# Kernel optimization log

Measured on AMD Instinct MI355X. Metric: run time of the kernel, lower is better.

## Reference

```python
import jax, jax.numpy as jnp
import numpy as np

INF = 1e8
SAMPLE_RATE = 22050.0
DOWNSAMPLE = 256.0
TARGET_RATE = SAMPLE_RATE / DOWNSAMPLE  # ~86.13 frames/sec
BEAT_RADIUS = 2.5
DOWNBEAT_RADIUS = 4.5
CLUSTERS = np.array([0.35, 0.7, 1.4, 2.8, 5.6], dtype=np.float64)

def _interval_length_ranges():
    # clusters_to_interval_length_ranges from the torch source
    edges = (CLUSTERS[:-1] + CLUSTERS[1:]) / 2.0
    ranges = [(-1.0, float(edges[0]))]
    for i in range(1, len(edges)):
        ranges.append((float(edges[i - 1]), float(edges[i])))
    ranges.append((float(edges[-1]), 1000.0))
    return ranges

RANGES = _interval_length_ranges()

def _assign_level(anchors, ann, stride, lo, hi):
    # anchors: [N] anchor points, ann: [M,3] (l, r, class)
    l = ann[:, 0][None, :]           # [1,M]
    r = ann[:, 1][None, :]           # [1,M]
    cls = ann[:, 2]                  # [M]
    radius = (cls == 0) * DOWNBEAT_RADIUS + (cls == 1) * BEAT_RADIUS
    a = anchors[:, None]             # [N,1]
    # non-centerness branch (centerness=False default)
    limit = l + radius[None, :] * stride
    in_sub = (a >= l) & (a <= jnp.minimum(r, limit))           # [N,M]
    l_star = a - l                                             # [N,M]
    r_star = r - a                                             # [N,M]
    max_lr = jnp.maximum(l_star, r_star)                       # [N,M]
    in_range = (max_lr >= lo) & (max_lr <= hi)                 # [N,M]
    areas = (ann[:, 1] - ann[:, 0])[None, :]                   # [1,M]
    area_mat = jnp.where(in_sub & in_range, areas, INF)        # [N,M]
    min_areas = jnp.min(area_mat, axis=1)                      # [N]
    idx = jnp.argmin(area_mat, axis=1)                         # [N]
    pos = min_areas != INF
    assigned = ann[idx]                                        # [N,3]
    assigned = assigned.at[:, 2].set(jnp.where(pos, assigned[:, 2], 0.0))
    norm_ann = assigned.at[:, :2].divide(stride)
    ls = jnp.take_along_axis(l_star, idx[:, None], axis=1)[:, 0]
    rs = jnp.take_along_axis(r_star, idx[:, None], axis=1)[:, 0]
    return pos, assigned, norm_ann, ls, rs, ls / stride, rs / stride

def setup_inputs() -> dict:
    key = jax.random.key(0)
    k1, k2, k3 = jax.random.split(key, 3)
    M = 256
    total_frames = 131072.0
    l = jnp.sort(jax.random.uniform(k1, (M,), minval=0.0, maxval=total_frames - 600.0))
    dur = jax.random.uniform(k2, (M,), minval=0.2, maxval=6.0) * TARGET_RATE
    r = l + dur
    cls = jax.random.randint(k3, (M,), 0, 2).astype(jnp.float32)
    ann = jnp.stack([l, r, cls], axis=1).astype(jnp.float32)
    Ns = [131072, 65536, 32768, 16384, 8192]
    anchors = {f"anchors{i}": (jnp.arange(n, dtype=jnp.float32) + 0.5) * (2.0 ** i)
               for i, n in enumerate(Ns)}
    return {"jth_annotations": ann, **anchors}

def reference(jth_annotations, anchors0, anchors1, anchors2, anchors3, anchors4):
    anchors_list = [anchors0, anchors1, anchors2, anchors3, anchors4]
    outs = []
    for i, anc in enumerate(anchors_list):
        stride = 2.0 ** i
        lo = RANGES[i][0] * TARGET_RATE
        hi = RANGES[i][1] * TARGET_RATE
        pos, assigned, norm_ann, ls, rs, nls, nrs = _assign_level(
            anc, jth_annotations, stride, lo, hi)
        levels = jnp.full(anc.shape, float(i + 1), dtype=anc.dtype)
        outs.append((pos, assigned, norm_ann, ls, rs, nls, nrs, levels))
    cat = lambda k: jnp.concatenate([o[k] for o in outs], axis=0)
    return (cat(0), cat(1), cat(2), cat(3), cat(4), cat(5), cat(6), cat(7))
```

## Files before the change

kernel.cpp:

```cpp
#include <hip/hip_runtime.h>


#define N_TOTAL 253952
#define INF_VAL 1.0e8f

__global__ __launch_bounds__(256) void assign_levels_v2(
    const float* __restrict__ ann,
    float* __restrict__ out)
{
    __shared__ float4 sA[256];
    __shared__ float  sL[256];
    __shared__ float  sC[256];

    const int b = blockIdx.x;
    int level, blockBase, gBase;
    float loC, hiC, stride;
    if (b < 128)      { level=0; blockBase=0;   gBase=0;      stride=1.0f;
                        loC=(float)(-1.0*86.1328125);  hiC=(float)(0.525*86.1328125); }
    else if (b < 192) { level=1; blockBase=128; gBase=131072; stride=2.0f;
                        loC=(float)(0.525*86.1328125); hiC=(float)(1.05*86.1328125); }
    else if (b < 224) { level=2; blockBase=192; gBase=196608; stride=4.0f;
                        loC=(float)(1.05*86.1328125);  hiC=(float)(2.1*86.1328125); }
    else if (b < 240) { level=3; blockBase=224; gBase=229376; stride=8.0f;
                        loC=(float)(2.1*86.1328125);   hiC=(float)(4.2*86.1328125); }
    else              { level=4; blockBase=240; gBase=245760; stride=16.0f;
                        loC=(float)(4.2*86.1328125);   hiC=(float)(1000.0*86.1328125); }

    const int t = threadIdx.x;
    {
        float l = ann[3*t+0], r = ann[3*t+1], c = ann[3*t+2];
        float radius = (c == 0.0f ? 4.5f : 0.0f) + (c == 1.0f ? 2.5f : 0.0f);
        float limit = l + radius * stride;
        sA[t] = make_float4(l, fminf(r, limit), r - l, r);
        sL[t] = l;
        sC[t] = c;
    }
    __syncthreads();

    const int i0 = (b - blockBase) * 1024 + t * 4;
    const float inv = 1.0f / stride;

    const float a0 = ((float)i0 + 0.5f) * stride;

    int cnt = 0;
    #pragma unroll
    for (int s = 128; s > 0; s >>= 1) {
        if (sL[cnt + s - 1] <= a0) cnt += s;
    }
    cnt += (sL[cnt < 256 ? cnt : 255] <= a0 && cnt < 256) ? 1 : 0;

    float ps[4], lb[4], rb[4], cl[4], lsv[4], rsv[4];

    #pragma unroll
    for (int k = 0; k < 4; ++k) {
        const float a = ((float)(i0 + k) + 0.5f) * stride;
        if (k) {
            while (cnt < 256 && sL[cnt] <= a) cnt++;
        }
        float best = INF_VAL;
        int bidx = 0;
        const float aMin = a - 520.0f;
        for (int j = cnt - 1; j >= 0; --j) {
            float4 q = sA[j];
            if (q.x < aMin) break;
            float l_ = a - q.x;
            float r_ = q.w - a;
            float mx = fmaxf(l_, r_);
            bool ok = (a <= q.y) & (mx >= loC) & (mx <= hiC);
            if (ok & (q.z <= best)) { best = q.z; bidx = j; }
        }
        const float4 qb = sA[bidx];
        const bool pos = best < INF_VAL;
        ps[k]  = pos ? 1.0f : 0.0f;
        lb[k]  = qb.x;
        rb[k]  = qb.w;
        cl[k]  = pos ? sC[bidx] : 0.0f;
        lsv[k] = a - qb.x;
        rsv[k] = qb.w - a;
    }

    const int g = gBase + i0;

    *(float4*)(out + g) = make_float4(ps[0], ps[1], ps[2], ps[3]);

    float* A = out + N_TOTAL + 3*g;
    *(float4*)(A + 0) = make_float4(lb[0], rb[0], cl[0], lb[1]);
    *(float4*)(A + 4) = make_float4(rb[1], cl[1], lb[2], rb[2]);
    *(float4*)(A + 8) = make_float4(cl[2], lb[3], rb[3], cl[3]);

    float* Nm = out + 4*N_TOTAL + 3*g;
    *(float4*)(Nm + 0) = make_float4(lb[0]*inv, rb[0]*inv, cl[0],     lb[1]*inv);
    *(float4*)(Nm + 4) = make_float4(rb[1]*inv, cl[1],     lb[2]*inv, rb[2]*inv);
    *(float4*)(Nm + 8) = make_float4(cl[2],     lb[3]*inv, rb[3]*inv, cl[3]);

    *(float4*)(out + 7*N_TOTAL  + g) = make_float4(lsv[0], lsv[1], lsv[2], lsv[3]);
    *(float4*)(out + 8*N_TOTAL  + g) = make_float4(rsv[0], rsv[1], rsv[2], rsv[3]);
    *(float4*)(out + 9*N_TOTAL  + g) = make_float4(lsv[0]*inv, lsv[1]*inv, lsv[2]*inv, lsv[3]*inv);
    *(float4*)(out + 10*N_TOTAL + g) = make_float4(rsv[0]*inv, rsv[1]*inv, rsv[2]*inv, rsv[3]*inv);

    const float lv = (float)(level + 1);
    *(float4*)(out + 11*N_TOTAL + g) = make_float4(lv, lv, lv, lv);
}

extern "C" void kernel_launch(void* const* d_in, const int* in_sizes, int n_in,
                              void* d_out, int out_size, void* d_ws, size_t ws_size,
                              hipStream_t stream) {
    const float* ann = (const float*)d_in[0];
    float* out = (float*)d_out;
    assign_levels_v2<<<248, 256, 0, stream>>>(ann, out);
}
```

Before: 12.43 us.

## Replace per-thread binary search with block-wide candidate window via syncthreads_count

```diff
diff --git a/kernel.cpp b/kernel.cpp
--- a/kernel.cpp
+++ b/kernel.cpp
@@ -4,12 +4,11 @@
 #define N_TOTAL 253952
 #define INF_VAL 1.0e8f
 
-__global__ __launch_bounds__(256) void assign_levels_v2(
+__global__ __launch_bounds__(256) void assign_levels_v3(
     const float* __restrict__ ann,
     float* __restrict__ out)
 {
     __shared__ float4 sA[256];
-    __shared__ float  sL[256];
     __shared__ float  sC[256];
 
     const int b = blockIdx.x;
@@ -27,56 +26,72 @@
                         loC=(float)(4.2*86.1328125);   hiC=(float)(1000.0*86.1328125); }
 
     const int t = threadIdx.x;
+    float l, r, c;
     {
-        float l = ann[3*t+0], r = ann[3*t+1], c = ann[3*t+2];
+        l = ann[3*t+0]; r = ann[3*t+1]; c = ann[3*t+2];
         float radius = (c == 0.0f ? 4.5f : 0.0f) + (c == 1.0f ? 2.5f : 0.0f);
         float limit = l + radius * stride;
         sA[t] = make_float4(l, fminf(r, limit), r - l, r);
-        sL[t] = l;
         sC[t] = c;
     }
-    __syncthreads();
 
-    const int i0 = (b - blockBase) * 1024 + t * 4;
+    const int firstIdx = (b - blockBase) * 1024;
+    const float aFirst = ((float)firstIdx + 0.5f) * stride;
+    const float aLast  = ((float)(firstIdx + 1023) + 0.5f) * stride;
+    const float aMinB = aFirst - 520.0f;
+
+    const int winLo = __syncthreads_count(l < aMinB);
+    const int winHi = __syncthreads_count(l <= aLast);
+
+    const int i0 = firstIdx + t * 4;
     const float inv = 1.0f / stride;
 
-    const float a0 = ((float)i0 + 0.5f) * stride;
+    const float a0 = ((float)(i0 + 0) + 0.5f) * stride;
+    const float a1 = ((float)(i0 + 1) + 0.5f) * stride;
+    const float a2 = ((float)(i0 + 2) + 0.5f) * stride;
+    const float a3 = ((float)(i0 + 3) + 0.5f) * stride;
 
-    int cnt = 0;
-    #pragma unroll
-    for (int s = 128; s > 0; s >>= 1) {
-        if (sL[cnt + s - 1] <= a0) cnt += s;
+    float best0 = INF_VAL, best1 = INF_VAL, best2 = INF_VAL, best3 = INF_VAL;
+    int   idx0 = 0, idx1 = 0, idx2 = 0, idx3 = 0;
+
+    for (int j = winLo; j < winHi; ++j) {
+        const float4 q = sA[j];
+        {
+            float mx = fmaxf(a0 - q.x, q.w - a0);
+            bool ok = (a0 >= q.x) & (a0 <= q.y) & (mx >= loC) & (mx <= hiC);
+            if (ok & (q.z < best0)) { best0 = q.z; idx0 = j; }
+        }
+        {
+            float mx = fmaxf(a1 - q.x, q.w - a1);
+            bool ok = (a1 >= q.x) & (a1 <= q.y) & (mx >= loC) & (mx <= hiC);
+            if (ok & (q.z < best1)) { best1 = q.z; idx1 = j; }
+        }
+        {
+            float mx = fmaxf(a2 - q.x, q.w - a2);
+            bool ok = (a2 >= q.x) & (a2 <= q.y) & (mx >= loC) & (mx <= hiC);
+            if (ok & (q.z < best2)) { best2 = q.z; idx2 = j; }
+        }
+        {
+            float mx = fmaxf(a3 - q.x, q.w - a3);
+            bool ok = (a3 >= q.x) & (a3 <= q.y) & (mx >= loC) & (mx <= hiC);
+            if (ok & (q.z < best3)) { best3 = q.z; idx3 = j; }
+        }
     }
-    cnt += (sL[cnt < 256 ? cnt : 255] <= a0 && cnt < 256) ? 1 : 0;
 
     float ps[4], lb[4], rb[4], cl[4], lsv[4], rsv[4];
-
+    const float aN[4] = {a0, a1, a2, a3};
+    const float bst[4] = {best0, best1, best2, best3};
+    const int   bix[4] = {idx0, idx1, idx2, idx3};
     #pragma unroll
     for (int k = 0; k < 4; ++k) {
-        const float a = ((float)(i0 + k) + 0.5f) * stride;
-        if (k) {
-            while (cnt < 256 && sL[cnt] <= a) cnt++;
-        }
-        float best = INF_VAL;
-        int bidx = 0;
-        const float aMin = a - 520.0f;
-        for (int j = cnt - 1; j >= 0; --j) {
-            float4 q = sA[j];
-            if (q.x < aMin) break;
-            float l_ = a - q.x;
-            float r_ = q.w - a;
-            float mx = fmaxf(l_, r_);
-            bool ok = (a <= q.y) & (mx >= loC) & (mx <= hiC);
-            if (ok & (q.z <= best)) { best = q.z; bidx = j; }
-        }
-        const float4 qb = sA[bidx];
-        const bool pos = best < INF_VAL;
+        const float4 qb = sA[bix[k]];
+        const bool pos = bst[k] < INF_VAL;
         ps[k]  = pos ? 1.0f : 0.0f;
         lb[k]  = qb.x;
         rb[k]  = qb.w;
-        cl[k]  = pos ? sC[bidx] : 0.0f;
-        lsv[k] = a - qb.x;
-        rsv[k] = qb.w - a;
+        cl[k]  = pos ? sC[bix[k]] : 0.0f;
+        lsv[k] = aN[k] - qb.x;
+        rsv[k] = qb.w - aN[k];
     }
 
     const int g = gBase + i0;
@@ -107,5 +122,5 @@
                               hipStream_t stream) {
     const float* ann = (const float*)d_in[0];
     float* out = (float*)d_out;
-    assign_levels_v2<<<248, 256, 0, stream>>>(ann, out);
+    assign_levels_v3<<<248, 256, 0, stream>>>(ann, out);
 }
```

After: 15.49 us. +24.6%, slower.
